# Kernel tuning notes

Measured on AMD Instinct MI355X. Metric: run time of the kernel, lower is better.

Reference implementation:

```python
import jax, jax.numpy as jnp
import numpy as np

N = 50000      # nodes
E = 400000     # edges (before self-loops)
D_IN = 128
HID = 128
D_OUT = 128
ED = 64        # edge feature dim
SLOPE_GAT = 0.2   # GATConv attention leaky_relu slope
SLOPE_ACT = 0.01  # nn.LeakyReLU default


def _init(key, shape, scale):
    return jax.random.normal(key, shape, dtype=jnp.float32) * scale


def setup_inputs() -> dict:
    key = jax.random.key(0)
    ks = iter(jax.random.split(key, 48))
    inp = {}
    inp["x"] = jax.random.normal(next(ks), (N, D_IN), dtype=jnp.float32)
    inp["edge_index"] = jax.random.randint(next(ks), (2, E), 0, N, dtype=jnp.int32)
    inp["edge_attr"] = jax.random.normal(next(ks), (E, ED), dtype=jnp.float32)
    # 3 GATConv layers (heads=1): lin_src weight, att_src, att_dst, lin_edge weight, att_edge, bias
    for l, din in enumerate([D_IN, HID, HID]):
        s = 1.0 / np.sqrt(din)
        inp[f"W{l}"] = _init(next(ks), (din, HID), s)
        inp[f"as{l}"] = _init(next(ks), (HID,), 0.1)
        inp[f"ad{l}"] = _init(next(ks), (HID,), 0.1)
        inp[f"We{l}"] = _init(next(ks), (ED, HID), 1.0 / np.sqrt(ED))
        inp[f"ae{l}"] = _init(next(ks), (HID,), 0.1)
        inp[f"b{l}"] = jnp.zeros((HID,), jnp.float32)
    inp["vn_w"] = jnp.zeros((HID,), jnp.float32)  # Embedding(1, hidden), init to 0
    sh = 1.0 / np.sqrt(HID)
    # VN MLP 1 (hidden->hidden->hidden) and final VN MLP (hidden->hidden->output)
    inp["m1w1"] = _init(next(ks), (HID, HID), sh); inp["m1b1"] = jnp.zeros((HID,), jnp.float32)
    inp["m1w2"] = _init(next(ks), (HID, HID), sh); inp["m1b2"] = jnp.zeros((HID,), jnp.float32)
    inp["m2w1"] = _init(next(ks), (HID, HID), sh); inp["m2b1"] = jnp.zeros((HID,), jnp.float32)
    inp["m2w2"] = _init(next(ks), (HID, D_OUT), sh); inp["m2b2"] = jnp.zeros((D_OUT,), jnp.float32)
    inp["Wout"] = _init(next(ks), (HID, D_OUT), sh); inp["bout"] = jnp.zeros((D_OUT,), jnp.float32)
    return inp


def _gat(h_in, src, dst, ea, W, a_s, a_d, We, a_e, b):
    """PyG GATConv (heads=1) on edges with self-loops already appended."""
    h = h_in @ W  # [N, HID]
    alpha = jax.nn.leaky_relu((h @ a_s)[src] + (h @ a_d)[dst] + (ea @ We) @ a_e, SLOPE_GAT)
    m = jax.ops.segment_max(alpha, dst, num_segments=N)
    ex = jnp.exp(alpha - m[dst])
    den = jax.ops.segment_sum(ex, dst, num_segments=N)
    coef = ex / den[dst]
    return jax.ops.segment_sum(coef[:, None] * h[src], dst, num_segments=N) + b


def reference(x, edge_index, edge_attr,
              W0, as0, ad0, We0, ae0, b0,
              W1, as1, ad1, We1, ae1, b1,
              W2, as2, ad2, We2, ae2, b2,
              vn_w, m1w1, m1b1, m1w2, m1b2, m2w1, m2b1, m2w2, m2b2,
              Wout, bout):
    src, dst = edge_index[0], edge_index[1]
    # add_self_loops(fill_value='mean'): self-loop edge_attr = mean of incoming edge_attr
    deg = jax.ops.segment_sum(jnp.ones((E,), jnp.float32), dst, num_segments=N)
    loop_attr = jax.ops.segment_sum(edge_attr, dst, num_segments=N) / jnp.maximum(deg, 1.0)[:, None]
    ar = jnp.arange(N, dtype=src.dtype)
    src2 = jnp.concatenate([src, ar])
    dst2 = jnp.concatenate([dst, ar])
    ea = jnp.concatenate([edge_attr, loop_attr], axis=0)

    out = _gat(x, src2, dst2, ea, W0, as0, ad0, We0, ae0, b0)  # no activation after initial
    out = jax.nn.leaky_relu(_gat(out, src2, dst2, ea, W1, as1, ad1, We1, ae1, b1), SLOPE_ACT)
    out = jax.nn.leaky_relu(_gat(out, src2, dst2, ea, W2, as2, ad2, We2, ae2, b2), SLOPE_ACT)

    # batch=None path: global_add_pool(out, None, size=1) + virtualnode_embedding(0)
    vn = jnp.sum(out, axis=0, keepdims=True) + vn_w[None, :]  # [1, HID]
    vn = jax.nn.relu(vn @ m1w1 + m1b1)
    vn = jax.nn.relu(vn @ m1w2 + m1b2)
    vn = jax.nn.relu(vn @ m2w1 + m2b1)
    vn = jax.nn.relu(vn @ m2w2 + m2b2)  # [1, D_OUT]

    node_out = out @ Wout + bout  # [N, D_OUT]
    return (node_out, vn)
```

## Files before the change

### kernel.cpp

```cpp
#include <hip/hip_runtime.h>

#define NN 50000
#define EE 400000
#define HID 128
#define ED 64
#define LDP 136
#define SLOTS 64

typedef __attribute__((ext_vector_type(8))) unsigned short ushort8_t;
typedef __attribute__((ext_vector_type(8))) short short8_t;
typedef __attribute__((ext_vector_type(4))) float f32x4;

static __device__ __forceinline__ unsigned short f2bf(float f) {
  unsigned u = __float_as_uint(f);
  unsigned r = (u + 0x7FFFu + ((u >> 16) & 1u)) >> 16;
  return (unsigned short)r;
}
static __device__ __forceinline__ float bf2f(unsigned short b) {
  return __uint_as_float((unsigned)b << 16);
}


__global__ __launch_bounds__(256) void k_misc(
    const float* __restrict__ x, unsigned short* __restrict__ xb,
    int* __restrict__ cnt, float* __restrict__ vnsum,
    const float* __restrict__ W0, const float* __restrict__ W1,
    const float* __restrict__ W2, const float* __restrict__ Wo,
    unsigned short* __restrict__ Wt, const float* __restrict__ We0,
    const float* __restrict__ We1, const float* __restrict__ We2,
    const float* __restrict__ ae0, const float* __restrict__ ae1,
    const float* __restrict__ ae2, float* __restrict__ weae) {
  int b = blockIdx.x;
  int t = threadIdx.x;
  if (b < 6250) {
    int i = b * 256 + t;
    float4 v = ((const float4*)x)[i];
    ushort4 o;
    o.x = f2bf(v.x); o.y = f2bf(v.y); o.z = f2bf(v.z); o.w = f2bf(v.w);
    ((ushort4*)xb)[i] = o;
  } else if (b < 6446) {
    int i = (b - 6250) * 256 + t;
    if (i < NN) cnt[i] = 0;
    if (b == 6250 && t < HID) vnsum[t] = 0.f;
  } else if (b < 6702) {
    int idx = (b - 6446) * 256 + t;
    int m = idx >> 14;
    int rem = idx & 16383;
    int k = rem >> 7;
    int n = rem & 127;
    const float* W = (m == 0) ? W0 : (m == 1) ? W1 : (m == 2) ? W2 : Wo;
    Wt[(size_t)m * 16384 + n * 128 + k] = f2bf(W[k * 128 + n]);
  } else {
    if (t >= 192) return;
    int l = t >> 6, j = t & 63;
    const float* We = (l == 0) ? We0 : (l == 1) ? We1 : We2;
    const float* ae = (l == 0) ? ae0 : (l == 1) ? ae1 : ae2;
    float acc = 0.f;
    for (int k = 0; k < HID; ++k) acc += We[j * HID + k] * ae[k];
    weae[l * ED + j] = acc;
  }
}

__global__ __launch_bounds__(256) void k_escscatter(
    const float* __restrict__ edge_attr, const float* __restrict__ weae,
    const int* __restrict__ src, const int* __restrict__ dst,
    int* __restrict__ cnt, float4* __restrict__ escv) {
  __shared__ float4 sw[3][16];
  int tid = threadIdx.x;
  if (tid < 48) ((float4*)sw)[tid] = ((const float4*)weae)[tid];
  __syncthreads();
  int c = tid & 15;
  int r0 = tid >> 4;
  float4 w0 = sw[0][c], w1 = sw[1][c], w2 = sw[2][c];
  float ra0[4], ra1[4], ra2[4];
  int rows[4];
#pragma unroll
  for (int pass = 0; pass < 4; ++pass) {
    int row = blockIdx.x * 64 + pass * 16 + r0;
    rows[pass] = row;
    float a0 = 0.f, a1 = 0.f, a2 = 0.f;
    if (row < EE) {
      float4 v = ((const float4*)edge_attr)[(size_t)row * 16 + c];
      a0 = v.x * w0.x + v.y * w0.y + v.z * w0.z + v.w * w0.w;
      a1 = v.x * w1.x + v.y * w1.y + v.z * w1.z + v.w * w1.w;
      a2 = v.x * w2.x + v.y * w2.y + v.z * w2.z + v.w * w2.w;
    }
#pragma unroll
    for (int o = 1; o < 16; o <<= 1) {
      a0 += __shfl_xor(a0, o, 64);
      a1 += __shfl_xor(a1, o, 64);
      a2 += __shfl_xor(a2, o, 64);
    }
    ra0[pass] = a0;
    ra1[pass] = a1;
    ra2[pass] = a2;
  }
  if (c == 0) {
    int dv[4], sv[4], p[4];
#pragma unroll
    for (int pass = 0; pass < 4; ++pass) {
      if (rows[pass] < EE) {
        dv[pass] = dst[rows[pass]];
        sv[pass] = src[rows[pass]];
      } else {
        dv[pass] = -1;
      }
    }
#pragma unroll
    for (int pass = 0; pass < 4; ++pass) {
      p[pass] = (dv[pass] >= 0) ? atomicAdd(&cnt[dv[pass]], 1) : SLOTS;
    }
#pragma unroll
    for (int pass = 0; pass < 4; ++pass) {
      if (dv[pass] >= 0 && p[pass] < SLOTS - 1) {
        escv[(size_t)dv[pass] * SLOTS + p[pass]] =
            make_float4(ra0[pass], ra1[pass], ra2[pass],
                        __int_as_float(sv[pass]));
      }
    }
  }
}


__global__ __launch_bounds__(256) void k_gemmA(
    const unsigned short* __restrict__ A, const unsigned short* __restrict__ Bt,
    const float* __restrict__ as_, const float* __restrict__ ad_,
    unsigned short* __restrict__ hb, float* __restrict__ hs,
    float* __restrict__ hd) {
  __shared__ unsigned short sA[64][LDP];
  __shared__ unsigned short sB[128][LDP];
  int tid = threadIdx.x;
  int row0 = blockIdx.x * 64;
  {
    int r = tid >> 2, sg = (tid & 3) * 32;
    int grow = row0 + r;
    const ushort8_t* src = (const ushort8_t*)(A + (size_t)grow * HID + sg);
    ushort8_t z = {0, 0, 0, 0, 0, 0, 0, 0};
#pragma unroll
    for (int i = 0; i < 4; ++i)
      *(ushort8_t*)&sA[r][sg + i * 8] = (grow < NN) ? src[i] : z;
  }
  {
    int r = tid >> 1, sg = (tid & 1) * 64;
    const ushort8_t* src = (const ushort8_t*)(Bt + r * HID + sg);
#pragma unroll
    for (int i = 0; i < 8; ++i) *(ushort8_t*)&sB[r][sg + i * 8] = src[i];
  }
  __syncthreads();
  int w = tid >> 6, l = tid & 63;
  int lr = l & 15, lg = l >> 4;
  f32x4 acc[8] = {};
  const unsigned short* pa = &sA[w * 16 + lr][lg * 8];
  const unsigned short* pb = &sB[lr][lg * 8];
#pragma unroll
  for (int ks = 0; ks < 4; ++ks) {
    short8_t a = *(const short8_t*)(pa + ks * 32);
#pragma unroll
    for (int ct = 0; ct < 8; ++ct) {
      short8_t b = *(const short8_t*)(pb + ct * 16 * LDP + ks * 32);
      acc[ct] = __builtin_amdgcn_mfma_f32_16x16x32_bf16(a, b, acc[ct], 0, 0, 0);
    }
  }
  int orow = row0 + w * 16 + lg * 4;
#pragma unroll
  for (int ct = 0; ct < 8; ++ct) {
    int col = ct * 16 + lr;
#pragma unroll
    for (int r = 0; r < 4; ++r) {
      int grow = orow + r;
      if (grow < NN) hb[(size_t)grow * HID + col] = f2bf(acc[ct][r]);
    }
  }
  float asv[8], adv[8];
#pragma unroll
  for (int ct = 0; ct < 8; ++ct) {
    asv[ct] = as_[ct * 16 + lr];
    adv[ct] = ad_[ct * 16 + lr];
  }
#pragma unroll
  for (int r = 0; r < 4; ++r) {
    float ps = 0.f, pd = 0.f;
#pragma unroll
    for (int ct = 0; ct < 8; ++ct) {
      ps += acc[ct][r] * asv[ct];
      pd += acc[ct][r] * adv[ct];
    }
#pragma unroll
    for (int o = 1; o < 16; o <<= 1) {
      ps += __shfl_xor(ps, o, 64);
      pd += __shfl_xor(pd, o, 64);
    }
    int grow = orow + r;
    if (lr == 0 && grow < NN) {
      hs[grow] = ps;
      hd[grow] = pd;
    }
  }
}

__global__ __launch_bounds__(256) void k_gemmO(
    const unsigned short* __restrict__ A, const unsigned short* __restrict__ Bt,
    const float* __restrict__ bias, float* __restrict__ O,
    float* __restrict__ vnsum) {
  __shared__ unsigned short sA[64][LDP];
  __shared__ unsigned short sB[128][LDP];
  int tid = threadIdx.x;
  int row0 = blockIdx.x * 64;
  {
    int r = tid >> 2, sg = (tid & 3) * 32;
    int grow = row0 + r;
    const ushort8_t* src = (const ushort8_t*)(A + (size_t)grow * HID + sg);
    ushort8_t z = {0, 0, 0, 0, 0, 0, 0, 0};
#pragma unroll
    for (int i = 0; i < 4; ++i)
      *(ushort8_t*)&sA[r][sg + i * 8] = (grow < NN) ? src[i] : z;
  }
  {
    int r = tid >> 1, sg = (tid & 1) * 64;
    const ushort8_t* src = (const ushort8_t*)(Bt + r * HID + sg);
#pragma unroll
    for (int i = 0; i < 8; ++i) *(ushort8_t*)&sB[r][sg + i * 8] = src[i];
  }
  __syncthreads();
  int w = tid >> 6, l = tid & 63;
  int lr = l & 15, lg = l >> 4;
  f32x4 acc[8] = {};
  const unsigned short* pa = &sA[w * 16 + lr][lg * 8];
  const unsigned short* pb = &sB[lr][lg * 8];
#pragma unroll
  for (int ks = 0; ks < 4; ++ks) {
    short8_t a = *(const short8_t*)(pa + ks * 32);
#pragma unroll
    for (int ct = 0; ct < 8; ++ct) {
      short8_t b = *(const short8_t*)(pb + ct * 16 * LDP + ks * 32);
      acc[ct] = __builtin_amdgcn_mfma_f32_16x16x32_bf16(a, b, acc[ct], 0, 0, 0);
    }
  }
  int orow = row0 + w * 16 + lg * 4;
#pragma unroll
  for (int ct = 0; ct < 8; ++ct) {
    int col = ct * 16 + lr;
    float bv = bias[col];
#pragma unroll
    for (int r = 0; r < 4; ++r) {
      int grow = orow + r;
      if (grow < NN) O[(size_t)grow * HID + col] = acc[ct][r] + bv;
    }
  }
  if (tid < HID) {
    float s = 0.f;
#pragma unroll
    for (int r = 0; r < 64; ++r) s += bf2f(sA[r][tid]);
    atomicAdd(&vnsum[tid], s);
  }
}


__global__ __launch_bounds__(256) void k_aggregate7(
    const unsigned short* __restrict__ hb, const float* __restrict__ hs,
    const float* __restrict__ hd, const float4* __restrict__ escv,
    const int* __restrict__ cnt, const float* __restrict__ bias,
    unsigned short* __restrict__ outb, int lsel, int act) {
  int i = blockIdx.x * 4 + (threadIdx.x >> 6);
  int lane = threadIdx.x & 63;
  if (i >= NN) return;
  int g = lane >> 4;
  int j = lane & 15;
  int deg = cnt[i];
  if (deg > SLOTS - 1) deg = SLOTS - 1;
  int nt = deg + 1;
  float hdi = hd[i];
  int t = lane;
  int sv = i;
  float esc_l = 0.f;
  if (t < deg) {
    float4 v = escv[(size_t)i * SLOTS + t];
    sv = __float_as_int(v.w);
    esc_l = (lsel == 0) ? v.x : (lsel == 1) ? v.y : v.z;
  }
  float se = esc_l;
#pragma unroll
  for (int o = 1; o < 64; o <<= 1) se += __shfl_xor(se, o, 64);
  float w = 0.f;
  if (t < nt) {
    float av;
    if (t < deg)
      av = hs[sv] + hdi + esc_l;
    else
      av = hs[i] + hdi + se / (float)(deg > 1 ? deg : 1);
    av = (av > 0.f) ? av : 0.2f * av;
    w = __expf(av);
  }
  float den_l = w;
  float4 acc0 = make_float4(0.f, 0.f, 0.f, 0.f);
  float4 acc1 = make_float4(0.f, 0.f, 0.f, 0.f);
  int q = g;
  if (q < nt) {
    float wq = __shfl(w, q, 64);
    int sq = __shfl(sv, q, 64);
    if (q == deg) sq = i;
    ushort8_t hv = *(const ushort8_t*)(hb + (size_t)sq * HID + j * 8);
    for (int qn = q + 4; qn < nt; qn += 4) {
      float wn = __shfl(w, qn, 64);
      int sn = __shfl(sv, qn, 64);
      if (qn == deg) sn = i;
      ushort8_t hn = *(const ushort8_t*)(hb + (size_t)sn * HID + j * 8);
      acc0.x += wq * bf2f(hv[0]);
      acc0.y += wq * bf2f(hv[1]);
      acc0.z += wq * bf2f(hv[2]);
      acc0.w += wq * bf2f(hv[3]);
      acc1.x += wq * bf2f(hv[4]);
      acc1.y += wq * bf2f(hv[5]);
      acc1.z += wq * bf2f(hv[6]);
      acc1.w += wq * bf2f(hv[7]);
      wq = wn;
      hv = hn;
    }
    acc0.x += wq * bf2f(hv[0]);
    acc0.y += wq * bf2f(hv[1]);
    acc0.z += wq * bf2f(hv[2]);
    acc0.w += wq * bf2f(hv[3]);
    acc1.x += wq * bf2f(hv[4]);
    acc1.y += wq * bf2f(hv[5]);
    acc1.z += wq * bf2f(hv[6]);
    acc1.w += wq * bf2f(hv[7]);
  }
#pragma unroll
  for (int o = 1; o < 64; o <<= 1) den_l += __shfl_xor(den_l, o, 64);
#pragma unroll
  for (int o = 16; o <= 32; o <<= 1) {
    acc0.x += __shfl_xor(acc0.x, o, 64);
    acc0.y += __shfl_xor(acc0.y, o, 64);
    acc0.z += __shfl_xor(acc0.z, o, 64);
    acc0.w += __shfl_xor(acc0.w, o, 64);
    acc1.x += __shfl_xor(acc1.x, o, 64);
    acc1.y += __shfl_xor(acc1.y, o, 64);
    acc1.z += __shfl_xor(acc1.z, o, 64);
    acc1.w += __shfl_xor(acc1.w, o, 64);
  }
  if (g == 0) {
    float inv = 1.f / den_l;
    const float4* bp = (const float4*)(bias + j * 8);
    float4 b0 = bp[0], b1 = bp[1];
    float v[8];
    v[0] = acc0.x * inv + b0.x; v[1] = acc0.y * inv + b0.y;
    v[2] = acc0.z * inv + b0.z; v[3] = acc0.w * inv + b0.w;
    v[4] = acc1.x * inv + b1.x; v[5] = acc1.y * inv + b1.y;
    v[6] = acc1.z * inv + b1.z; v[7] = acc1.w * inv + b1.w;
    ushort8_t ob;
#pragma unroll
    for (int q2 = 0; q2 < 8; ++q2) {
      float tv = v[q2];
      if (act) tv = (tv > 0.f) ? tv : 0.01f * tv;
      ob[q2] = f2bf(tv);
    }
    *(ushort8_t*)(outb + (size_t)i * HID + j * 8) = ob;
  }
}


__global__ void k_mlp(const float* __restrict__ vnsum, const float* __restrict__ vn_w,
                      const float* __restrict__ w1, const float* __restrict__ b1,
                      const float* __restrict__ w2, const float* __restrict__ b2,
                      const float* __restrict__ w3, const float* __restrict__ b3,
                      const float* __restrict__ w4, const float* __restrict__ b4,
                      float* __restrict__ outv) {
  __shared__ float xb[HID], yb[HID];
  int t = threadIdx.x;
  xb[t] = vnsum[t] + vn_w[t];
  __syncthreads();
  const float* Ws[4] = {w1, w2, w3, w4};
  const float* Bs[4] = {b1, b2, b3, b4};
  float* cur = xb;
  float* nxt = yb;
  for (int l = 0; l < 4; ++l) {
    const float* W = Ws[l];
    const float* B = Bs[l];
    float acc = B[t];
    for (int d = 0; d < HID; ++d) acc += cur[d] * W[d * HID + t];
    nxt[t] = fmaxf(acc, 0.f);
    __syncthreads();
    float* tmp = cur; cur = nxt; nxt = tmp;
  }
  outv[t] = cur[t];
}


extern "C" void kernel_launch(void* const* d_in, const int* in_sizes, int n_in,
                              void* d_out, int out_size, void* d_ws, size_t ws_size,
                              hipStream_t stream) {
  const float* x = (const float*)d_in[0];
  const int* ei = (const int*)d_in[1];
  const float* edge_attr = (const float*)d_in[2];
  const float *W[3], *as_[3], *ad_[3], *We[3], *ae[3], *bb[3];
  for (int l = 0; l < 3; ++l) {
    W[l]   = (const float*)d_in[3 + l * 6 + 0];
    as_[l] = (const float*)d_in[3 + l * 6 + 1];
    ad_[l] = (const float*)d_in[3 + l * 6 + 2];
    We[l]  = (const float*)d_in[3 + l * 6 + 3];
    ae[l]  = (const float*)d_in[3 + l * 6 + 4];
    bb[l]  = (const float*)d_in[3 + l * 6 + 5];
  }
  const float* vn_w = (const float*)d_in[21];
  const float* m1w1 = (const float*)d_in[22];
  const float* m1b1 = (const float*)d_in[23];
  const float* m1w2 = (const float*)d_in[24];
  const float* m1b2 = (const float*)d_in[25];
  const float* m2w1 = (const float*)d_in[26];
  const float* m2b1 = (const float*)d_in[27];
  const float* m2w2 = (const float*)d_in[28];
  const float* m2b2 = (const float*)d_in[29];
  const float* Wout = (const float*)d_in[30];
  const float* bout = (const float*)d_in[31];

  char* ws = (char*)d_ws;
  size_t o = 0;
  auto alloc = [&](size_t bytes) {
    o = (o + 255) & ~(size_t)255;
    void* p = ws + o;
    o += bytes;
    return p;
  };
  unsigned short* xb   = (unsigned short*)alloc((size_t)NN * HID * 2);
  unsigned short* hb   = (unsigned short*)alloc((size_t)NN * HID * 2);
  unsigned short* outb = (unsigned short*)alloc((size_t)NN * HID * 2);
  unsigned short* Wtb  = (unsigned short*)alloc((size_t)4 * HID * HID * 2);
  float4* escv   = (float4*)alloc((size_t)NN * SLOTS * 16);
  float* hs     = (float*)alloc((size_t)NN * 4);
  float* hd     = (float*)alloc((size_t)NN * 4);
  float* vnsum  = (float*)alloc(HID * 4);
  float* weae   = (float*)alloc(3 * ED * 4);
  int* cnt      = (int*)alloc((size_t)NN * 4);

  const int* srcv = ei;
  const int* dstv = ei + EE;

  k_misc<<<6703, 256, 0, stream>>>(x, xb, cnt, vnsum, W[0], W[1], W[2], Wout,
                                   Wtb, We[0], We[1], We[2], ae[0], ae[1],
                                   ae[2], weae);
  k_escscatter<<<(EE + 63) / 64, 256, 0, stream>>>(edge_attr, weae, srcv, dstv,
                                                   cnt, escv);

  const unsigned short* in_b = xb;
  for (int l = 0; l < 3; ++l) {
    k_gemmA<<<(NN + 63) / 64, 256, 0, stream>>>(
        in_b, Wtb + (size_t)l * HID * HID, as_[l], ad_[l], hb, hs, hd);
    k_aggregate7<<<(NN + 3) / 4, 256, 0, stream>>>(
        hb, hs, hd, escv, cnt, bb[l], outb, l, (l > 0) ? 1 : 0);
    in_b = outb;
  }

  float* node_out = (float*)d_out;
  k_gemmO<<<(NN + 63) / 64, 256, 0, stream>>>(
      outb, Wtb + (size_t)3 * HID * HID, bout, node_out, vnsum);
  k_mlp<<<1, 128, 0, stream>>>(vnsum, vn_w, m1w1, m1b1, m1w2, m1b2, m2w1, m2b1,
                               m2w2, m2b2, node_out + (size_t)NN * HID);
}
```

Baseline: 232.2 us.

## Shrink init kernel, fuse conversions into scatter kernel, fold MLP into gemmO

The first kernel now only zeroes counters and computes the We·ae projections. The x and weight bf16 conversions move into the edge scatter kernel, so they run concurrently with the atomic scatter work. The separate single-block virtual-node MLP kernel is removed: the last gemmO block, found through a done counter with threadfence, runs the MLP. This cuts kernel launches and tail gaps, at the cost of a serialized MLP tail inside one block and an extra global atomic per block.

```diff
diff --git a/kernel.cpp b/kernel.cpp
--- a/kernel.cpp
+++ b/kernel.cpp
@@ -21,35 +21,20 @@
 }
 
 
-__global__ __launch_bounds__(256) void k_misc(
-    const float* __restrict__ x, unsigned short* __restrict__ xb,
-    int* __restrict__ cnt, float* __restrict__ vnsum,
-    const float* __restrict__ W0, const float* __restrict__ W1,
-    const float* __restrict__ W2, const float* __restrict__ Wo,
-    unsigned short* __restrict__ Wt, const float* __restrict__ We0,
-    const float* __restrict__ We1, const float* __restrict__ We2,
-    const float* __restrict__ ae0, const float* __restrict__ ae1,
-    const float* __restrict__ ae2, float* __restrict__ weae) {
+__global__ __launch_bounds__(256) void k_init(
+    int* __restrict__ cnt, float* __restrict__ vnsum, int* __restrict__ done,
+    const float* __restrict__ We0, const float* __restrict__ We1,
+    const float* __restrict__ We2, const float* __restrict__ ae0,
+    const float* __restrict__ ae1, const float* __restrict__ ae2,
+    float* __restrict__ weae) {
   int b = blockIdx.x;
   int t = threadIdx.x;
-  if (b < 6250) {
+  if (b < 196) {
     int i = b * 256 + t;
-    float4 v = ((const float4*)x)[i];
-    ushort4 o;
-    o.x = f2bf(v.x); o.y = f2bf(v.y); o.z = f2bf(v.z); o.w = f2bf(v.w);
-    ((ushort4*)xb)[i] = o;
-  } else if (b < 6446) {
-    int i = (b - 6250) * 256 + t;
     if (i < NN) cnt[i] = 0;
-    if (b == 6250 && t < HID) vnsum[t] = 0.f;
-  } else if (b < 6702) {
-    int idx = (b - 6446) * 256 + t;
-    int m = idx >> 14;
-    int rem = idx & 16383;
-    int k = rem >> 7;
-    int n = rem & 127;
-    const float* W = (m == 0) ? W0 : (m == 1) ? W1 : (m == 2) ? W2 : Wo;
-    Wt[(size_t)m * 16384 + n * 128 + k] = f2bf(W[k * 128 + n]);
+  } else if (b == 196) {
+    if (t < HID) vnsum[t] = 0.f;
+    if (t == 128) done[0] = 0;
   } else {
     if (t >= 192) return;
     int l = t >> 6, j = t & 63;
@@ -61,63 +46,85 @@
   }
 }
 
-__global__ __launch_bounds__(256) void k_escscatter(
+
+__global__ __launch_bounds__(256) void k_main(
     const float* __restrict__ edge_attr, const float* __restrict__ weae,
     const int* __restrict__ src, const int* __restrict__ dst,
-    int* __restrict__ cnt, float4* __restrict__ escv) {
-  __shared__ float4 sw[3][16];
+    int* __restrict__ cnt, float4* __restrict__ escv,
+    const float* __restrict__ x, unsigned short* __restrict__ xb,
+    const float* __restrict__ W0, const float* __restrict__ W1,
+    const float* __restrict__ W2, const float* __restrict__ Wo,
+    unsigned short* __restrict__ Wt) {
+  int b = blockIdx.x;
   int tid = threadIdx.x;
-  if (tid < 48) ((float4*)sw)[tid] = ((const float4*)weae)[tid];
-  __syncthreads();
-  int c = tid & 15;
-  int r0 = tid >> 4;
-  float4 w0 = sw[0][c], w1 = sw[1][c], w2 = sw[2][c];
-  float ra0[4], ra1[4], ra2[4];
-  int rows[4];
-#pragma unroll
-  for (int pass = 0; pass < 4; ++pass) {
-    int row = blockIdx.x * 64 + pass * 16 + r0;
-    rows[pass] = row;
-    float a0 = 0.f, a1 = 0.f, a2 = 0.f;
-    if (row < EE) {
-      float4 v = ((const float4*)edge_attr)[(size_t)row * 16 + c];
-      a0 = v.x * w0.x + v.y * w0.y + v.z * w0.z + v.w * w0.w;
-      a1 = v.x * w1.x + v.y * w1.y + v.z * w1.z + v.w * w1.w;
-      a2 = v.x * w2.x + v.y * w2.y + v.z * w2.z + v.w * w2.w;
-    }
-#pragma unroll
-    for (int o = 1; o < 16; o <<= 1) {
-      a0 += __shfl_xor(a0, o, 64);
-      a1 += __shfl_xor(a1, o, 64);
-      a2 += __shfl_xor(a2, o, 64);
-    }
-    ra0[pass] = a0;
-    ra1[pass] = a1;
-    ra2[pass] = a2;
-  }
-  if (c == 0) {
-    int dv[4], sv[4], p[4];
+  if (b < 6250) {
+    __shared__ float4 sw[3][16];
+    if (tid < 48) ((float4*)sw)[tid] = ((const float4*)weae)[tid];
+    __syncthreads();
+    int c = tid & 15;
+    int r0 = tid >> 4;
+    float4 w0 = sw[0][c], w1 = sw[1][c], w2 = sw[2][c];
+    float ra0[4], ra1[4], ra2[4];
+    int rows[4];
 #pragma unroll
     for (int pass = 0; pass < 4; ++pass) {
-      if (rows[pass] < EE) {
-        dv[pass] = dst[rows[pass]];
-        sv[pass] = src[rows[pass]];
-      } else {
-        dv[pass] = -1;
+      int row = b * 64 + pass * 16 + r0;
+      rows[pass] = row;
+      float a0 = 0.f, a1 = 0.f, a2 = 0.f;
+      if (row < EE) {
+        float4 v = ((const float4*)edge_attr)[(size_t)row * 16 + c];
+        a0 = v.x * w0.x + v.y * w0.y + v.z * w0.z + v.w * w0.w;
+        a1 = v.x * w1.x + v.y * w1.y + v.z * w1.z + v.w * w1.w;
+        a2 = v.x * w2.x + v.y * w2.y + v.z * w2.z + v.w * w2.w;
       }
-    }
-#pragma unroll
-    for (int pass = 0; pass < 4; ++pass) {
-      p[pass] = (dv[pass] >= 0) ? atomicAdd(&cnt[dv[pass]], 1) : SLOTS;
-    }
-#pragma unroll
-    for (int pass = 0; pass < 4; ++pass) {
-      if (dv[pass] >= 0 && p[pass] < SLOTS - 1) {
-        escv[(size_t)dv[pass] * SLOTS + p[pass]] =
-            make_float4(ra0[pass], ra1[pass], ra2[pass],
-                        __int_as_float(sv[pass]));
+#pragma unroll
+      for (int o = 1; o < 16; o <<= 1) {
+        a0 += __shfl_xor(a0, o, 64);
+        a1 += __shfl_xor(a1, o, 64);
+        a2 += __shfl_xor(a2, o, 64);
       }
-    }
+      ra0[pass] = a0;
+      ra1[pass] = a1;
+      ra2[pass] = a2;
+    }
+    if (c == 0) {
+      int dv[4], sv[4], p[4];
+#pragma unroll
+      for (int pass = 0; pass < 4; ++pass) {
+        if (rows[pass] < EE) {
+          dv[pass] = dst[rows[pass]];
+          sv[pass] = src[rows[pass]];
+        } else {
+          dv[pass] = -1;
+        }
+      }
+#pragma unroll
+      for (int pass = 0; pass < 4; ++pass) {
+        p[pass] = (dv[pass] >= 0) ? atomicAdd(&cnt[dv[pass]], 1) : SLOTS;
+      }
+#pragma unroll
+      for (int pass = 0; pass < 4; ++pass) {
+        if (dv[pass] >= 0 && p[pass] < SLOTS - 1) {
+          escv[(size_t)dv[pass] * SLOTS + p[pass]] =
+              make_float4(ra0[pass], ra1[pass], ra2[pass],
+                          __int_as_float(sv[pass]));
+        }
+      }
+    }
+  } else if (b < 12500) {
+    int i = (b - 6250) * 256 + tid;
+    float4 v = ((const float4*)x)[i];
+    ushort4 o;
+    o.x = f2bf(v.x); o.y = f2bf(v.y); o.z = f2bf(v.z); o.w = f2bf(v.w);
+    ((ushort4*)xb)[i] = o;
+  } else {
+    int idx = (b - 12500) * 256 + tid;
+    int m = idx >> 14;
+    int rem = idx & 16383;
+    int k = rem >> 7;
+    int n = rem & 127;
+    const float* W = (m == 0) ? W0 : (m == 1) ? W1 : (m == 2) ? W2 : Wo;
+    Wt[(size_t)m * 16384 + n * 128 + k] = f2bf(W[k * 128 + n]);
   }
 }
 
@@ -201,9 +208,15 @@
 __global__ __launch_bounds__(256) void k_gemmO(
     const unsigned short* __restrict__ A, const unsigned short* __restrict__ Bt,
     const float* __restrict__ bias, float* __restrict__ O,
-    float* __restrict__ vnsum) {
+    float* __restrict__ vnsum, int* __restrict__ done,
+    const float* __restrict__ vn_w, const float* __restrict__ w1,
+    const float* __restrict__ b1, const float* __restrict__ w2,
+    const float* __restrict__ b2, const float* __restrict__ w3,
+    const float* __restrict__ b3, const float* __restrict__ w4,
+    const float* __restrict__ b4, float* __restrict__ outv) {
   __shared__ unsigned short sA[64][LDP];
   __shared__ unsigned short sB[128][LDP];
+  __shared__ int lastflag;
   int tid = threadIdx.x;
   int row0 = blockIdx.x * 64;
   {
@@ -253,6 +266,29 @@
     for (int r = 0; r < 64; ++r) s += bf2f(sA[r][tid]);
     atomicAdd(&vnsum[tid], s);
   }
+  __threadfence();
+  __syncthreads();
+  if (tid == 0) lastflag = (atomicAdd(done, 1) == (int)gridDim.x - 1) ? 1 : 0;
+  __syncthreads();
+  if (!lastflag) return;
+  float* mb0 = (float*)&sA[0][0];
+  float* mb1 = mb0 + HID;
+  if (tid < HID) mb0[tid] = atomicAdd(&vnsum[tid], 0.f) + vn_w[tid];
+  __syncthreads();
+  const float* Ws[4] = {w1, w2, w3, w4};
+  const float* Bs[4] = {b1, b2, b3, b4};
+#pragma unroll
+  for (int ml = 0; ml < 4; ++ml) {
+    float* cur = (ml & 1) ? mb1 : mb0;
+    float* nxt = (ml & 1) ? mb0 : mb1;
+    if (tid < HID) {
+      float a = Bs[ml][tid];
+      for (int d = 0; d < HID; ++d) a += cur[d] * Ws[ml][d * HID + tid];
+      nxt[tid] = fmaxf(a, 0.f);
+    }
+    __syncthreads();
+  }
+  if (tid < HID) outv[tid] = mb0[tid];
 }
 
 
@@ -359,33 +395,6 @@
 }
 
 
-__global__ void k_mlp(const float* __restrict__ vnsum, const float* __restrict__ vn_w,
-                      const float* __restrict__ w1, const float* __restrict__ b1,
-                      const float* __restrict__ w2, const float* __restrict__ b2,
-                      const float* __restrict__ w3, const float* __restrict__ b3,
-                      const float* __restrict__ w4, const float* __restrict__ b4,
-                      float* __restrict__ outv) {
-  __shared__ float xb[HID], yb[HID];
-  int t = threadIdx.x;
-  xb[t] = vnsum[t] + vn_w[t];
-  __syncthreads();
-  const float* Ws[4] = {w1, w2, w3, w4};
-  const float* Bs[4] = {b1, b2, b3, b4};
-  float* cur = xb;
-  float* nxt = yb;
-  for (int l = 0; l < 4; ++l) {
-    const float* W = Ws[l];
-    const float* B = Bs[l];
-    float acc = B[t];
-    for (int d = 0; d < HID; ++d) acc += cur[d] * W[d * HID + t];
-    nxt[t] = fmaxf(acc, 0.f);
-    __syncthreads();
-    float* tmp = cur; cur = nxt; nxt = tmp;
-  }
-  outv[t] = cur[t];
-}
-
-
 extern "C" void kernel_launch(void* const* d_in, const int* in_sizes, int n_in,
                               void* d_out, int out_size, void* d_ws, size_t ws_size,
                               hipStream_t stream) {
@@ -431,15 +440,15 @@
   float* vnsum  = (float*)alloc(HID * 4);
   float* weae   = (float*)alloc(3 * ED * 4);
   int* cnt      = (int*)alloc((size_t)NN * 4);
+  int* done     = (int*)alloc(256);
 
   const int* srcv = ei;
   const int* dstv = ei + EE;
 
-  k_misc<<<6703, 256, 0, stream>>>(x, xb, cnt, vnsum, W[0], W[1], W[2], Wout,
-                                   Wtb, We[0], We[1], We[2], ae[0], ae[1],
-                                   ae[2], weae);
-  k_escscatter<<<(EE + 63) / 64, 256, 0, stream>>>(edge_attr, weae, srcv, dstv,
-                                                   cnt, escv);
+  k_init<<<198, 256, 0, stream>>>(cnt, vnsum, done, We[0], We[1], We[2], ae[0],
+                                  ae[1], ae[2], weae);
+  k_main<<<12756, 256, 0, stream>>>(edge_attr, weae, srcv, dstv, cnt, escv, x,
+                                    xb, W[0], W[1], W[2], Wout, Wtb);
 
   const unsigned short* in_b = xb;
   for (int l = 0; l < 3; ++l) {
@@ -452,7 +461,7 @@
 
   float* node_out = (float*)d_out;
   k_gemmO<<<(NN + 63) / 64, 256, 0, stream>>>(
-      outb, Wtb + (size_t)3 * HID * HID, bout, node_out, vnsum);
-  k_mlp<<<1, 128, 0, stream>>>(vnsum, vn_w, m1w1, m1b1, m1w2, m1b2, m2w1, m2b1,
-                               m2w2, m2b2, node_out + (size_t)NN * HID);
-}
+      outb, Wtb + (size_t)3 * HID * HID, bout, node_out, vnsum, done, vn_w,
+      m1w1, m1b1, m1w2, m1b2, m2w1, m2b1, m2w2, m2b2,
+      node_out + (size_t)NN * HID);
+}
```

Measured after the change: 275.5 us. +18.7%, slower.
